# Optimization experiments

Hardware: AMD Instinct MI355X
Metric: run time of the kernel (lower is better)

The kernel has to match this reference:

```python
import jax, jax.numpy as jnp
import numpy as np

N = 16384   # number of nodes == output_dim
E = 524288  # directed edges (avg degree 32)
IN_DIM, HID = 16, 128


def _glorot(key, shape):
    fan_in = shape[0]
    return jax.random.normal(key, shape, dtype=jnp.float32) / jnp.sqrt(jnp.float32(fan_in))


def setup_inputs() -> dict:
    key = jax.random.key(0)
    ks = jax.random.split(key, 6)
    x = jax.random.normal(ks[0], (N, IN_DIM), dtype=jnp.float32)
    edge_index = jax.random.randint(ks[1], (2, E), 0, N, dtype=jnp.int64)
    return {
        "x": x,
        "edge_index": edge_index,
        "W1": _glorot(ks[2], (IN_DIM, HID)), "b1": jnp.zeros((HID,), jnp.float32),
        "W2": _glorot(ks[3], (HID, HID)),    "b2": jnp.zeros((HID,), jnp.float32),
        "W3": _glorot(ks[4], (HID, HID)),    "b3": jnp.zeros((HID,), jnp.float32),
        "Wfc": _glorot(ks[5], (HID, N)),     "bfc": jnp.zeros((N,), jnp.float32),
    }


def _gcn_conv(x, W, b, src, dst, norm):
    # GCNConv: h = D^{-1/2} (A + I) D^{-1/2} (x @ W) + b
    h = x @ W                              # [N, out]
    msg = h[src] * norm[:, None]           # gather + per-edge scale
    agg = jax.ops.segment_sum(msg, dst, num_segments=N)  # scatter-add to targets
    return agg + b


def reference(x, edge_index, W1, b1, W2, b2, W3, b3, Wfc, bfc):
    # Add self-loops (PyG GCNConv default)
    loop = jnp.arange(N, dtype=edge_index.dtype)
    src = jnp.concatenate([edge_index[0], loop])   # [E+N]
    dst = jnp.concatenate([edge_index[1], loop])
    # Symmetric degree normalization: deg over incoming edges (weight 1)
    deg = jax.ops.segment_sum(jnp.ones_like(dst, dtype=jnp.float32), dst, num_segments=N)
    dinv = jnp.where(deg > 0, jax.lax.rsqrt(deg), 0.0)
    norm = dinv[src] * dinv[dst]                   # [E+N]

    h = jax.nn.relu(_gcn_conv(x, W1, b1, src, dst, norm))
    h = jax.nn.relu(_gcn_conv(h, W2, b2, src, dst, norm))
    h = jax.nn.relu(_gcn_conv(h, W3, b3, src, dst, norm))
    return h @ Wfc + bfc                           # [N, N] logits over nodes
```

## Files before the change

kernel.cpp:

```cpp
#include <hip/hip_runtime.h>

#define N_NODES 16384
#define E_EDGES 524288
#define HID 128
#define LDSTR 132

typedef __attribute__((ext_vector_type(8))) short bf16x8;
typedef __attribute__((ext_vector_type(4))) float f32x4;

__device__ __forceinline__ unsigned short f2bf(float x) {
    unsigned u = __builtin_bit_cast(unsigned, x);
    u = u + 0x7fff + ((u >> 16) & 1);
    return (unsigned short)(u >> 16);
}
__device__ __forceinline__ float bf2f(unsigned short h) {
    return __builtin_bit_cast(float, (unsigned)h << 16);
}


__global__ __launch_bounds__(256) void k_zero(int* __restrict__ cnt) {
    int i = blockIdx.x * 256 + threadIdx.x;
    if (i < N_NODES) cnt[i] = 0;
}

__global__ __launch_bounds__(256) void k_count(const int* __restrict__ ei, int* __restrict__ cnt) {
    int e = blockIdx.x * 256 + threadIdx.x;
    if (e < E_EDGES) {
        int d = ei[E_EDGES + e];
        atomicAdd(&cnt[d], 1);
    }
}

__global__ __launch_bounds__(1024) void k_scan(const int* __restrict__ cnt, int* __restrict__ rp,
                                               int* __restrict__ cur, float* __restrict__ dinv) {
    __shared__ int part[1024];
    int t = threadIdx.x;
    int base = t * 16;
    int loc[16];
    int s = 0;
#pragma unroll
    for (int i = 0; i < 16; ++i) { loc[i] = cnt[base + i]; s += loc[i]; }
    part[t] = s;
    __syncthreads();
    for (int off = 1; off < 1024; off <<= 1) {
        int add = (t >= off) ? part[t - off] : 0;
        __syncthreads();
        part[t] += add;
        __syncthreads();
    }
    int excl = (t == 0) ? 0 : part[t - 1];
#pragma unroll
    for (int i = 0; i < 16; ++i) {
        rp[base + i] = excl;
        cur[base + i] = excl;
        dinv[base + i] = rsqrtf((float)(loc[i] + 1));
        excl += loc[i];
    }
    if (t == 1023) rp[N_NODES] = excl;
}

__global__ __launch_bounds__(256) void k_fill(const int* __restrict__ ei, int* __restrict__ cur,
                                              int* __restrict__ eidx) {
    int e = blockIdx.x * 256 + threadIdx.x;
    if (e < E_EDGES) {
        int s = ei[e];
        int d = ei[E_EDGES + e];
        int p = atomicAdd(&cur[d], 1);
        eidx[p] = s;
    }
}


__global__ __launch_bounds__(256) void k_gemm16(const float* __restrict__ X, const float* __restrict__ W,
                                                float* __restrict__ T) {
    __shared__ float sW[16 * 128];
    int t = threadIdx.x;
#pragma unroll
    for (int i = 0; i < 8; ++i) sW[i * 256 + t] = W[i * 256 + t];
    __syncthreads();
    int row = blockIdx.x * 2 + (t >> 7);
    int c = t & 127;
    const float* xr = X + row * 16;
    float acc = 0.f;
#pragma unroll
    for (int k = 0; k < 16; ++k) acc = fmaf(xr[k], sW[k * 128 + c], acc);
    T[row * HID + c] = acc;
}

__global__ __launch_bounds__(256) void k_gemm128(const float* __restrict__ A, const float* __restrict__ W,
                                                 float* __restrict__ T) {
    __shared__ float sA[64][132];
    __shared__ float sW[128][132];
    int t = threadIdx.x;
    int bm = blockIdx.x * 64;
#pragma unroll
    for (int it = 0; it < 8; ++it) {
        int f = it * 256 + t;
        int m = f >> 5, k4 = f & 31;
        *(float4*)(&sA[m][k4 * 4]) = *(const float4*)(A + (bm + m) * HID + k4 * 4);
    }
#pragma unroll
    for (int it = 0; it < 16; ++it) {
        int f = it * 256 + t;
        int k = f >> 5, n4 = f & 31;
        *(float4*)(&sW[k][n4 * 4]) = *(const float4*)(W + k * HID + n4 * 4);
    }
    __syncthreads();
    int tx = t & 15, ty = t >> 4;
    float acc[4][8] = {};
    for (int k4 = 0; k4 < 32; ++k4) {
        float4 a[4], b0[4], b1[4];
#pragma unroll
        for (int i = 0; i < 4; ++i) a[i] = *(const float4*)(&sA[ty * 4 + i][k4 * 4]);
#pragma unroll
        for (int kk = 0; kk < 4; ++kk) {
            b0[kk] = *(const float4*)(&sW[k4 * 4 + kk][tx * 4]);
            b1[kk] = *(const float4*)(&sW[k4 * 4 + kk][tx * 4 + 64]);
        }
#pragma unroll
        for (int kk = 0; kk < 4; ++kk) {
#pragma unroll
            for (int i = 0; i < 4; ++i) {
                float av = reinterpret_cast<const float*>(&a[i])[kk];
#pragma unroll
                for (int j = 0; j < 4; ++j) {
                    acc[i][j]     = fmaf(av, reinterpret_cast<const float*>(&b0[kk])[j], acc[i][j]);
                    acc[i][4 + j] = fmaf(av, reinterpret_cast<const float*>(&b1[kk])[j], acc[i][4 + j]);
                }
            }
        }
    }
#pragma unroll
    for (int i = 0; i < 4; ++i) {
        int row = bm + ty * 4 + i;
        float4 o0, o1;
        o0.x = acc[i][0]; o0.y = acc[i][1]; o0.z = acc[i][2]; o0.w = acc[i][3];
        o1.x = acc[i][4]; o1.y = acc[i][5]; o1.z = acc[i][6]; o1.w = acc[i][7];
        *(float4*)(T + row * HID + tx * 4) = o0;
        *(float4*)(T + row * HID + tx * 4 + 64) = o1;
    }
}

__global__ __launch_bounds__(128) void k_agg(const float* __restrict__ T, const int* __restrict__ rp,
                                             const int* __restrict__ eidx, const float* __restrict__ dinv,
                                             const float* __restrict__ b, float* __restrict__ H) {
    __shared__ int se[128];
    __shared__ float sw[128];
    int i = blockIdx.x;
    int c = threadIdx.x;
    float di = dinv[i];
    float acc = di * T[i * HID + c];
    int beg = rp[i], end = rp[i + 1];
    for (int base = beg; base < end; base += 128) {
        int e = base + c;
        if (e < end) {
            int s = eidx[e];
            se[c] = s;
            sw[c] = dinv[s];
        }
        __syncthreads();
        int n = min(128, end - base);
        for (int j = 0; j < n; ++j) {
            acc += sw[j] * T[se[j] * HID + c];
        }
        __syncthreads();
    }
    float v = fmaf(di, acc, b[c]);
    H[i * HID + c] = fmaxf(v, 0.0f);
}


__global__ __launch_bounds__(256) void k_split_a(const float* __restrict__ A,
                                                 unsigned short* __restrict__ hi,
                                                 unsigned short* __restrict__ lo) {
    int i = (blockIdx.x * 256 + threadIdx.x) * 8;
    float4 v0 = *(const float4*)(A + i);
    float4 v1 = *(const float4*)(A + i + 4);
    float v[8] = {v0.x, v0.y, v0.z, v0.w, v1.x, v1.y, v1.z, v1.w};
    alignas(16) unsigned short hb[8], lb[8];
#pragma unroll
    for (int j = 0; j < 8; ++j) {
        unsigned short h = f2bf(v[j]);
        hb[j] = h;
        lb[j] = f2bf(v[j] - bf2f(h));
    }
    *(uint4*)(hi + i) = *(uint4*)hb;
    *(uint4*)(lo + i) = *(uint4*)lb;
}

__global__ __launch_bounds__(256) void k_split_b(const float* __restrict__ W,
                                                 unsigned short* __restrict__ bhi,
                                                 unsigned short* __restrict__ blo) {
    __shared__ float sm[32][132];
    int t = threadIdx.x;
    int nb = blockIdx.x;
    int kb = blockIdx.y;
#pragma unroll
    for (int i = 0; i < 4; ++i) {
        int idx = i * 256 + t;
        int k = idx >> 5, n4 = idx & 31;
        *(float4*)(&sm[k][n4 * 4]) =
            *(const float4*)(W + (size_t)(kb * 32 + k) * N_NODES + nb * 128 + n4 * 4);
    }
    __syncthreads();
    int n = t >> 1, half = t & 1;
    alignas(16) unsigned short hb[16], lb[16];
#pragma unroll
    for (int j = 0; j < 16; ++j) {
        float x = sm[half * 16 + j][n];
        unsigned short h = f2bf(x);
        hb[j] = h;
        lb[j] = f2bf(x - bf2f(h));
    }
    size_t o = (size_t)(nb * 128 + n) * 128 + kb * 32 + half * 16;
    *(uint4*)(bhi + o) = *(uint4*)hb;
    *(uint4*)(bhi + o + 8) = *(uint4*)(hb + 8);
    *(uint4*)(blo + o) = *(uint4*)lb;
    *(uint4*)(blo + o + 8) = *(uint4*)(lb + 8);
}

__global__ __launch_bounds__(256, 1) void k_fc_mfma(const unsigned short* __restrict__ Ahi,
                                                    const unsigned short* __restrict__ Alo,
                                                    const unsigned short* __restrict__ Bhi,
                                                    const unsigned short* __restrict__ Blo,
                                                    const float* __restrict__ bias,
                                                    float* __restrict__ C) {
    __shared__ unsigned short sAhi[128 * LDSTR];
    __shared__ unsigned short sAlo[128 * LDSTR];
    __shared__ unsigned short sBhi[128 * LDSTR];
    __shared__ unsigned short sBlo[128 * LDSTR];
    int t = threadIdx.x;
    int bn = blockIdx.x, bm = blockIdx.y;

    {
        const unsigned short* g0 = Ahi + (size_t)bm * 128 * 128;
        const unsigned short* g1 = Alo + (size_t)bm * 128 * 128;
        const unsigned short* g2 = Bhi + (size_t)bn * 128 * 128;
        const unsigned short* g3 = Blo + (size_t)bn * 128 * 128;
#pragma unroll
        for (int it = 0; it < 8; ++it) {
            int c = it * 256 + t;
            int r = c >> 4, ko = (c & 15) * 8;
            *(uint4*)(sAhi + r * LDSTR + ko) = *(const uint4*)(g0 + r * 128 + ko);
            *(uint4*)(sAlo + r * LDSTR + ko) = *(const uint4*)(g1 + r * 128 + ko);
            *(uint4*)(sBhi + r * LDSTR + ko) = *(const uint4*)(g2 + r * 128 + ko);
            *(uint4*)(sBlo + r * LDSTR + ko) = *(const uint4*)(g3 + r * 128 + ko);
        }
    }
    __syncthreads();

    int wid = t >> 6, lane = t & 63;
    int wm = wid >> 1, wn = wid & 1;
    int row16 = lane & 15, kq = lane >> 4;

    f32x4 acc[4][4] = {};
#pragma unroll
    for (int ks = 0; ks < 4; ++ks) {
        bf16x8 ah[4], al[4], bh[4], bl[4];
        int ko = ks * 32 + kq * 8;
#pragma unroll
        for (int m = 0; m < 4; ++m) {
            int r = wm * 64 + m * 16 + row16;
            ah[m] = *(const bf16x8*)(sAhi + r * LDSTR + ko);
            al[m] = *(const bf16x8*)(sAlo + r * LDSTR + ko);
        }
#pragma unroll
        for (int n = 0; n < 4; ++n) {
            int r = wn * 64 + n * 16 + row16;
            bh[n] = *(const bf16x8*)(sBhi + r * LDSTR + ko);
            bl[n] = *(const bf16x8*)(sBlo + r * LDSTR + ko);
        }
#pragma unroll
        for (int m = 0; m < 4; ++m)
#pragma unroll
            for (int n = 0; n < 4; ++n) {
                acc[m][n] = __builtin_amdgcn_mfma_f32_16x16x32_bf16(ah[m], bh[n], acc[m][n], 0, 0, 0);
                acc[m][n] = __builtin_amdgcn_mfma_f32_16x16x32_bf16(ah[m], bl[n], acc[m][n], 0, 0, 0);
                acc[m][n] = __builtin_amdgcn_mfma_f32_16x16x32_bf16(al[m], bh[n], acc[m][n], 0, 0, 0);
            }
    }

#pragma unroll
    for (int n = 0; n < 4; ++n) {
        int col = bn * 128 + wn * 64 + n * 16 + row16;
        float bv = bias[col];
#pragma unroll
        for (int m = 0; m < 4; ++m) {
            int r0 = bm * 128 + wm * 64 + m * 16 + kq * 4;
#pragma unroll
            for (int r = 0; r < 4; ++r)
                C[(size_t)(r0 + r) * N_NODES + col] = acc[m][n][r] + bv;
        }
    }
}


extern "C" void kernel_launch(void* const* d_in, const int* in_sizes, int n_in,
                              void* d_out, int out_size, void* d_ws, size_t ws_size,
                              hipStream_t stream) {
    const float* x   = (const float*)d_in[0];
    const int*   ei  = (const int*)d_in[1];
    const float* W1  = (const float*)d_in[2];
    const float* b1  = (const float*)d_in[3];
    const float* W2  = (const float*)d_in[4];
    const float* b2  = (const float*)d_in[5];
    const float* W3  = (const float*)d_in[6];
    const float* b3  = (const float*)d_in[7];
    const float* Wfc = (const float*)d_in[8];
    const float* bfc = (const float*)d_in[9];
    float* out = (float*)d_out;

    char* ws = (char*)d_ws;
    int* cnt  = (int*)ws;
    int* rp   = cnt + N_NODES;
    int* cur  = rp + N_NODES + 64;
    int* eidx = cur + N_NODES;
    float* dinv = (float*)(eidx + E_EDGES);
    float* t  = dinv + N_NODES;
    float* h  = t + N_NODES * HID;
    unsigned short* ahi = (unsigned short*)t;
    unsigned short* alo = ahi + N_NODES * HID;
    unsigned short* bhi = (unsigned short*)(h + N_NODES * HID);
    unsigned short* blo = bhi + N_NODES * HID;

    k_zero<<<N_NODES / 256, 256, 0, stream>>>(cnt);
    k_count<<<E_EDGES / 256, 256, 0, stream>>>(ei, cnt);
    k_scan<<<1, 1024, 0, stream>>>(cnt, rp, cur, dinv);
    k_fill<<<E_EDGES / 256, 256, 0, stream>>>(ei, cur, eidx);

    k_gemm16<<<N_NODES / 2, 256, 0, stream>>>(x, W1, t);
    k_agg<<<N_NODES, 128, 0, stream>>>(t, rp, eidx, dinv, b1, h);
    k_gemm128<<<N_NODES / 64, 256, 0, stream>>>(h, W2, t);
    k_agg<<<N_NODES, 128, 0, stream>>>(t, rp, eidx, dinv, b2, h);
    k_gemm128<<<N_NODES / 64, 256, 0, stream>>>(h, W3, t);
    k_agg<<<N_NODES, 128, 0, stream>>>(t, rp, eidx, dinv, b3, h);

    k_split_b<<<dim3(N_NODES / 128, HID / 32), 256, 0, stream>>>(Wfc, bhi, blo);
    k_split_a<<<(N_NODES * HID) / (256 * 8), 256, 0, stream>>>(h, ahi, alo);

    k_fc_mfma<<<dim3(N_NODES / 128, N_NODES / 128), 256, 0, stream>>>(ahi, alo, bhi, blo, bfc, out);
}
```

Measured before the change: 638.8 us.

## Load FC GEMM operands directly from global memory, drop LDS staging, nontemporal stores

The final [N,N] FC GEMM no longer stages the hi/lo bf16 A and B tiles into 132 KB of shared memory. Each wave now reads its MFMA fragments straight from global memory and relies on L1/L2 for reuse. This removes the LDS copy and barrier and lifts the one-block-per-CU occupancy limit. The output is written with nontemporal stores to avoid polluting cache with the 1 GB result. The trade-off is redundant global and L2 traffic for operands that waves in the same block share.

```diff
diff --git a/kernel.cpp b/kernel.cpp
--- a/kernel.cpp
+++ b/kernel.cpp
@@ -3,7 +3,6 @@
 #define N_NODES 16384
 #define E_EDGES 524288
 #define HID 128
-#define LDSTR 132
 
 typedef __attribute__((ext_vector_type(8))) short bf16x8;
 typedef __attribute__((ext_vector_type(4))) float f32x4;
@@ -219,77 +218,60 @@
     *(uint4*)(blo + o + 8) = *(uint4*)(lb + 8);
 }
 
-__global__ __launch_bounds__(256, 1) void k_fc_mfma(const unsigned short* __restrict__ Ahi,
-                                                    const unsigned short* __restrict__ Alo,
-                                                    const unsigned short* __restrict__ Bhi,
-                                                    const unsigned short* __restrict__ Blo,
-                                                    const float* __restrict__ bias,
-                                                    float* __restrict__ C) {
-    __shared__ unsigned short sAhi[128 * LDSTR];
-    __shared__ unsigned short sAlo[128 * LDSTR];
-    __shared__ unsigned short sBhi[128 * LDSTR];
-    __shared__ unsigned short sBlo[128 * LDSTR];
-    int t = threadIdx.x;
-    int bn = blockIdx.x, bm = blockIdx.y;
-
-    {
-        const unsigned short* g0 = Ahi + (size_t)bm * 128 * 128;
-        const unsigned short* g1 = Alo + (size_t)bm * 128 * 128;
-        const unsigned short* g2 = Bhi + (size_t)bn * 128 * 128;
-        const unsigned short* g3 = Blo + (size_t)bn * 128 * 128;
-#pragma unroll
-        for (int it = 0; it < 8; ++it) {
-            int c = it * 256 + t;
-            int r = c >> 4, ko = (c & 15) * 8;
-            *(uint4*)(sAhi + r * LDSTR + ko) = *(const uint4*)(g0 + r * 128 + ko);
-            *(uint4*)(sAlo + r * LDSTR + ko) = *(const uint4*)(g1 + r * 128 + ko);
-            *(uint4*)(sBhi + r * LDSTR + ko) = *(const uint4*)(g2 + r * 128 + ko);
-            *(uint4*)(sBlo + r * LDSTR + ko) = *(const uint4*)(g3 + r * 128 + ko);
-        }
-    }
-    __syncthreads();
-
+__global__ __launch_bounds__(256) void k_fc_mfma(const unsigned short* __restrict__ Ahi,
+                                                 const unsigned short* __restrict__ Alo,
+                                                 const unsigned short* __restrict__ Bhi,
+                                                 const unsigned short* __restrict__ Blo,
+                                                 const float* __restrict__ bias,
+                                                 float* __restrict__ C) {
+    int t = threadIdx.x;
     int wid = t >> 6, lane = t & 63;
     int wm = wid >> 1, wn = wid & 1;
     int row16 = lane & 15, kq = lane >> 4;
+    int m0 = blockIdx.y * 128 + wm * 64;
+    int n0 = blockIdx.x * 128 + wn * 64;
+
+    const unsigned short* pah = Ahi + (size_t)(m0 + row16) * HID + kq * 8;
+    const unsigned short* pal = Alo + (size_t)(m0 + row16) * HID + kq * 8;
+    const unsigned short* pbh = Bhi + (size_t)(n0 + row16) * HID + kq * 8;
+    const unsigned short* pbl = Blo + (size_t)(n0 + row16) * HID + kq * 8;
 
     f32x4 acc[4][4] = {};
 #pragma unroll
     for (int ks = 0; ks < 4; ++ks) {
-        bf16x8 ah[4], al[4], bh[4], bl[4];
-        int ko = ks * 32 + kq * 8;
+        bf16x8 ah[4], al[4];
 #pragma unroll
         for (int m = 0; m < 4; ++m) {
-            int r = wm * 64 + m * 16 + row16;
-            ah[m] = *(const bf16x8*)(sAhi + r * LDSTR + ko);
-            al[m] = *(const bf16x8*)(sAlo + r * LDSTR + ko);
+            ah[m] = *(const bf16x8*)(pah + m * 16 * HID + ks * 32);
+            al[m] = *(const bf16x8*)(pal + m * 16 * HID + ks * 32);
         }
 #pragma unroll
         for (int n = 0; n < 4; ++n) {
-            int r = wn * 64 + n * 16 + row16;
-            bh[n] = *(const bf16x8*)(sBhi + r * LDSTR + ko);
-            bl[n] = *(const bf16x8*)(sBlo + r * LDSTR + ko);
-        }
-#pragma unroll
-        for (int m = 0; m < 4; ++m)
-#pragma unroll
-            for (int n = 0; n < 4; ++n) {
-                acc[m][n] = __builtin_amdgcn_mfma_f32_16x16x32_bf16(ah[m], bh[n], acc[m][n], 0, 0, 0);
-                acc[m][n] = __builtin_amdgcn_mfma_f32_16x16x32_bf16(ah[m], bl[n], acc[m][n], 0, 0, 0);
-                acc[m][n] = __builtin_amdgcn_mfma_f32_16x16x32_bf16(al[m], bh[n], acc[m][n], 0, 0, 0);
-            }
+            bf16x8 bh = *(const bf16x8*)(pbh + n * 16 * HID + ks * 32);
+            bf16x8 bl = *(const bf16x8*)(pbl + n * 16 * HID + ks * 32);
+#pragma unroll
+            for (int m = 0; m < 4; ++m)
+                acc[m][n] = __builtin_amdgcn_mfma_f32_16x16x32_bf16(ah[m], bh, acc[m][n], 0, 0, 0);
+#pragma unroll
+            for (int m = 0; m < 4; ++m)
+                acc[m][n] = __builtin_amdgcn_mfma_f32_16x16x32_bf16(ah[m], bl, acc[m][n], 0, 0, 0);
+#pragma unroll
+            for (int m = 0; m < 4; ++m)
+                acc[m][n] = __builtin_amdgcn_mfma_f32_16x16x32_bf16(al[m], bh, acc[m][n], 0, 0, 0);
+        }
     }
 
 #pragma unroll
     for (int n = 0; n < 4; ++n) {
-        int col = bn * 128 + wn * 64 + n * 16 + row16;
+        int col = n0 + n * 16 + row16;
         float bv = bias[col];
 #pragma unroll
         for (int m = 0; m < 4; ++m) {
-            int r0 = bm * 128 + wm * 64 + m * 16 + kq * 4;
+            int r0 = m0 + m * 16 + kq * 4;
 #pragma unroll
             for (int r = 0; r < 4; ++r)
-                C[(size_t)(r0 + r) * N_NODES + col] = acc[m][n][r] + bv;
+                __builtin_nontemporal_store(acc[m][n][r] + bv,
+                                            C + (size_t)(r0 + r) * N_NODES + col);
         }
     }
 }
```

Measured after the change: 704.1 us. 1.1x slower.
